# Optimization experiments

Measured on AMD Instinct MI355X. Metric: run time of the kernel, lower is better.

The kernel has to match this reference:

```python
import jax, jax.numpy as jnp
import numpy as np

DIM = 384
HEADS = 12
W = 7  # window_size
N = W * W
B = 4096

def _relative_position_index(ws):
    ch = np.arange(ws)
    coords = np.stack(np.meshgrid(ch, ch, indexing='ij'))  # [2, W, W]
    cf = coords.reshape(2, -1)  # [2, W*W]
    rel = cf[:, :, None] - cf[:, None, :]  # [2, N, N]
    rel = rel.transpose(1, 2, 0)
    rel[:, :, 0] += ws - 1
    rel[:, :, 1] += ws - 1
    rel[:, :, 0] *= 2 * ws - 1
    return rel.sum(-1).astype(np.int32)  # [N, N]

def setup_inputs() -> dict:
    key = jax.random.key(0)
    ks = jax.random.split(key, 8)
    s = 0.02
    return {
        'x': jax.random.normal(ks[0], (B, N, DIM), jnp.float32),
        'y': jax.random.normal(ks[1], (B, N, DIM), jnp.float32),
        'q_w': jax.random.normal(ks[2], (DIM, DIM), jnp.float32) * s,
        'q_b': jnp.zeros((DIM,), jnp.float32),
        'kv_w': jax.random.normal(ks[3], (2 * DIM, DIM), jnp.float32) * s,
        'kv_b': jnp.zeros((2 * DIM,), jnp.float32),
        'proj_w': jax.random.normal(ks[4], (DIM, DIM), jnp.float32) * s,
        'proj_b': jnp.zeros((DIM,), jnp.float32),
        'rel_table': jax.random.normal(ks[5], ((2 * W - 1) ** 2, HEADS), jnp.float32) * s,
        'rel_index': jnp.asarray(_relative_position_index(W)),
    }

def reference(x, y, q_w, q_b, kv_w, kv_b, proj_w, proj_b, rel_table, rel_index):
    Bx, N1, C = x.shape
    N2 = y.shape[1]
    hd = C // HEADS
    scale = hd ** -0.5
    # projections (torch Linear: x @ W^T + b)
    q = (x @ q_w.T + q_b).reshape(Bx, N1, HEADS, hd)
    kv = (y @ kv_w.T + kv_b).reshape(Bx, N2, 2, HEADS, hd)
    k = kv[:, :, 0]  # [B, N2, H, d]
    v = kv[:, :, 1]
    attn = jnp.einsum('bqhd,bkhd->bhqk', q, k) * scale
    # relative position bias: [N1, N2, H] -> [H, N1, N2]
    bias = rel_table[rel_index.reshape(-1)].reshape(N1, N2, HEADS)
    attn = attn + jnp.transpose(bias, (2, 0, 1))[None]
    attn = jax.nn.softmax(attn, axis=-1)
    out = jnp.einsum('bhqk,bkhd->bqhd', attn, v).reshape(Bx, N1, C)
    return out @ proj_w.T + proj_b
```

## Files before the change

### kernel.cpp

```cpp
#include <hip/hip_runtime.h>

#define DIM 384
#define HEADS 12
#define HD 32
#define NTOK 49
#define NWIN 4096
#define MTOT (NWIN*NTOK)
#define PSTR 72

typedef __attribute__((ext_vector_type(8))) __bf16 bf16x8;
typedef __attribute__((ext_vector_type(4))) float f32x4;

static __device__ __forceinline__ f32x4 mfma16(bf16x8 a, bf16x8 b, f32x4 c) {
  return __builtin_amdgcn_mfma_f32_16x16x32_bf16(a, b, c, 0, 0, 0);
}

static __device__ __forceinline__ void gload_lds16(const void* g, void* l) {
  __builtin_amdgcn_global_load_lds(
      (const __attribute__((address_space(1))) unsigned int*)g,
      (__attribute__((address_space(3))) unsigned int*)l, 16, 0, 0);
}

__global__ void k_prep(const float* __restrict__ qw, const float* __restrict__ kvw,
                       const float* __restrict__ pw, const float* __restrict__ rel_table,
                       const int* __restrict__ rel_index,
                       __bf16* __restrict__ qw_bf, __bf16* __restrict__ kvw_bf,
                       __bf16* __restrict__ pw_bf, float* __restrict__ bias_pad) {
  int i = blockIdx.x * 256 + threadIdx.x;
  if (i < DIM*DIM)   qw_bf[i] = (__bf16)qw[i];
  if (i < 2*DIM*DIM) kvw_bf[i] = (__bf16)kvw[i];
  if (i < DIM*DIM)   pw_bf[i] = (__bf16)pw[i];
  if (i < HEADS*64*64) {
    int h = i >> 12, rem = i & 4095, q = rem >> 6, k = rem & 63;
    float v;
    if (k >= NTOK)      v = -1e30f;
    else if (q >= NTOK) v = 0.0f;
    else v = rel_table[rel_index[q*NTOK + k] * HEADS + h];
    bias_pad[i] = v;
  }
}

__global__ __launch_bounds__(256) void k_cvt(const float* __restrict__ x,
                                             const float* __restrict__ y,
                                             __bf16* __restrict__ xb,
                                             __bf16* __restrict__ yb) {
  const size_t NCH = (size_t)MTOT * DIM / 8;
  size_t i = (size_t)blockIdx.x * 256 + threadIdx.x;
  size_t stride = (size_t)gridDim.x * 256;
  for (; i < 2*NCH; i += stride) {
    const float* s; __bf16* d; size_t c;
    if (i < NCH) { s = x; d = xb; c = i; } else { s = y; d = yb; c = i - NCH; }
    float4 v0 = *(const float4*)(s + c*8);
    float4 v1 = *(const float4*)(s + c*8 + 4);
    bf16x8 t;
    t[0]=(__bf16)v0.x; t[1]=(__bf16)v0.y; t[2]=(__bf16)v0.z; t[3]=(__bf16)v0.w;
    t[4]=(__bf16)v1.x; t[5]=(__bf16)v1.y; t[6]=(__bf16)v1.z; t[7]=(__bf16)v1.w;
    *(bf16x8*)(d + c*8) = t;
  }
}

__global__ __launch_bounds__(256, 4) void k_qkv(
    const __bf16* __restrict__ xb, const __bf16* __restrict__ yb,
    const __bf16* __restrict__ qw_bf, const __bf16* __restrict__ kvw_bf,
    const float* __restrict__ q_b, const float* __restrict__ kv_b,
    __bf16* __restrict__ Qws, __bf16* __restrict__ Kws, __bf16* __restrict__ Vws)
{
  int b = blockIdx.x;
  int orig = (b & 7) * 1764 + (b >> 3);
  int mtile = orig / 9;
  int nt9 = orig - mtile*9;
  const __bf16* A; const __bf16* Bw; const float* bias; __bf16* Cout;
  int wrow0, col0;
  if (nt9 < 3) { A = xb; Bw = qw_bf; bias = q_b; Cout = Qws; wrow0 = nt9*128; col0 = wrow0; }
  else {
    A = yb; Bw = kvw_bf; bias = kv_b; wrow0 = (nt9-3)*128;
    if (wrow0 < DIM) { Cout = Kws; col0 = wrow0; } else { Cout = Vws; col0 = wrow0 - DIM; }
  }
  bias += wrow0;

  __shared__ __align__(16) __bf16 As[2][128*32];
  __shared__ __align__(16) __bf16 Bs[2][128*32];

  int t = threadIdx.x, lane = t & 63, wave = t >> 6;
  int l15 = lane & 15, g = lane >> 4;
  int wr = (wave >> 1) * 64, wc = (wave & 1) * 64;
  int row0b = mtile*128;

  int sr  = 2*(lane >> 3) + ((lane >> 2) & 1);
  int scb = (lane & 3) ^ ((lane >> 3) & 3);
  const __bf16* asrc[2]; const __bf16* bsrc[2];
  #pragma unroll
  for (int j = 0; j < 2; ++j) {
    int ar = (wave*2 + j)*16 + sr;
    asrc[j] = A  + (size_t)(row0b + ar)*DIM + scb*8;
    bsrc[j] = Bw + (size_t)(wrow0 + ar)*DIM + scb*8;
  }

  f32x4 acc[4][4];
  #pragma unroll
  for (int a=0;a<4;a++)
    #pragma unroll
    for (int bb=0;bb<4;bb++) acc[a][bb] = (f32x4){0.f,0.f,0.f,0.f};

  #pragma unroll
  for (int j = 0; j < 2; ++j) {
    gload_lds16(asrc[j], (char*)&As[0][0] + (wave*2+j)*1024);
    gload_lds16(bsrc[j], (char*)&Bs[0][0] + (wave*2+j)*1024);
  }
  __syncthreads();

  int lslot = l15*64 + ((g ^ ((l15 >> 1) & 3)) << 4);

  int buf = 0;
  #pragma unroll 2
  for (int kt = 0; kt < 12; ++kt) {
    if (kt < 11) {
      int kk = (kt+1)*32;
      #pragma unroll
      for (int j = 0; j < 2; ++j) {
        gload_lds16(asrc[j] + kk, (char*)&As[buf^1][0] + (wave*2+j)*1024);
        gload_lds16(bsrc[j] + kk, (char*)&Bs[buf^1][0] + (wave*2+j)*1024);
      }
    }
    bf16x8 af[4], bfv[4];
    #pragma unroll
    for (int a=0;a<4;a++)
      af[a]  = *(const bf16x8*)((const char*)&As[buf][0] + (wr + a*16)*64 + lslot);
    #pragma unroll
    for (int bb=0;bb<4;bb++)
      bfv[bb] = *(const bf16x8*)((const char*)&Bs[buf][0] + (wc + bb*16)*64 + lslot);
    #pragma unroll
    for (int a=0;a<4;a++)
      #pragma unroll
      for (int bb=0;bb<4;bb++)
        acc[a][bb] = mfma16(af[a], bfv[bb], acc[a][bb]);
    __syncthreads();
    buf ^= 1;
  }

  #pragma unroll
  for (int a=0;a<4;a++) {
    #pragma unroll
    for (int bb=0;bb<4;bb++) {
      int colw = wc + bb*16 + l15;
      float bi = bias[colw];
      size_t cbase = (size_t)(row0b + wr + a*16 + 4*g)*DIM + (col0 + colw);
      #pragma unroll
      for (int r=0;r<4;r++)
        Cout[cbase + (size_t)r*DIM] = (__bf16)(acc[a][bb][r] + bi);
    }
  }
}

__global__ __launch_bounds__(256) void k_attn(
    __bf16* qao,
    const __bf16* __restrict__ Kws, const __bf16* __restrict__ Vws,
    const float* __restrict__ bias_pad)
{
  __shared__ __align__(16) __bf16 Psh[4][64*PSTR];
  __shared__ __align__(16) __bf16 VTsh[4][32*PSTR];
  int b = blockIdx.x;
  int lane = threadIdx.x & 63, wave = threadIdx.x >> 6;
  int l15 = lane & 15, g = lane >> 4;
  __bf16* Pw  = Psh[wave];
  __bf16* VTw = VTsh[wave];
  size_t rowbase = (size_t)b * NTOK * DIM;
  const float scale = 0.17677669529663687f;

  for (int e = lane; e < 32*15; e += 64) {
    int d = e / 15, k = 49 + (e - d*15);
    VTw[d*PSTR + k] = (__bf16)0.0f;
  }

  for (int hh = 0; hh < 3; hh++) {
    int h = wave + hh*4;
    for (int e = lane; e < NTOK*HD; e += 64) {
      int k = e >> 5, d = e & 31;
      VTw[d*PSTR + k] = Vws[rowbase + (size_t)k*DIM + h*HD + d];
    }
    bf16x8 qf[4], kf[4];
    #pragma unroll
    for (int mt=0; mt<4; mt++) {
      int q = 16*mt + l15; if (q > 48) q = 48;
      qf[mt] = *(const bf16x8*)(qao + rowbase + (size_t)q*DIM + h*HD + g*8);
    }
    #pragma unroll
    for (int nt=0; nt<4; nt++) {
      int kk = 16*nt + l15; if (kk > 48) kk = 48;
      kf[nt] = *(const bf16x8*)(Kws + rowbase + (size_t)kk*DIM + h*HD + g*8);
    }
    f32x4 sacc[4][4];
    #pragma unroll
    for (int mt=0; mt<4; mt++)
      #pragma unroll
      for (int nt=0; nt<4; nt++)
        sacc[mt][nt] = mfma16(qf[mt], kf[nt], (f32x4){0.f,0.f,0.f,0.f});

    const float* bt = bias_pad + h*4096;
    float rs[4][4];
    #pragma unroll
    for (int mt=0; mt<4; mt++) {
      #pragma unroll
      for (int r=0; r<4; r++) {
        int q = 16*mt + 4*g + r;
        float v0 = sacc[mt][0][r]*scale + bt[q*64 +  0 + l15];
        float v1 = sacc[mt][1][r]*scale + bt[q*64 + 16 + l15];
        float v2 = sacc[mt][2][r]*scale + bt[q*64 + 32 + l15];
        float v3 = sacc[mt][3][r]*scale + bt[q*64 + 48 + l15];
        float m = fmaxf(fmaxf(v0,v1), fmaxf(v2,v3));
        #pragma unroll
        for (int off=1; off<16; off<<=1) m = fmaxf(m, __shfl_xor(m, off));
        v0 = __expf(v0-m); v1 = __expf(v1-m); v2 = __expf(v2-m); v3 = __expf(v3-m);
        float s = v0+v1+v2+v3;
        #pragma unroll
        for (int off=1; off<16; off<<=1) s += __shfl_xor(s, off);
        rs[mt][r] = s;
        Pw[q*PSTR +  0 + l15] = (__bf16)v0;
        Pw[q*PSTR + 16 + l15] = (__bf16)v1;
        Pw[q*PSTR + 32 + l15] = (__bf16)v2;
        Pw[q*PSTR + 48 + l15] = (__bf16)v3;
      }
    }

    #pragma unroll
    for (int mt=0; mt<4; mt++) {
      #pragma unroll
      for (int dt=0; dt<2; dt++) {
        f32x4 o = (f32x4){0.f,0.f,0.f,0.f};
        #pragma unroll
        for (int ks=0; ks<2; ks++) {
          bf16x8 pa = *(const bf16x8*)(Pw  + (16*mt + l15)*PSTR + 32*ks + 8*g);
          bf16x8 vb = *(const bf16x8*)(VTw + (16*dt + l15)*PSTR + 32*ks + 8*g);
          o = mfma16(pa, vb, o);
        }
        #pragma unroll
        for (int r=0; r<4; r++) {
          int q = 16*mt + 4*g + r;
          if (q < NTOK)
            qao[rowbase + (size_t)q*DIM + h*HD + 16*dt + l15] = (__bf16)(o[r] / rs[mt][r]);
        }
      }
    }
  }
}

__global__ __launch_bounds__(256, 4) void k_proj(
    const __bf16* __restrict__ Aao, const __bf16* __restrict__ pw_bf,
    const float* __restrict__ pb, float* __restrict__ out)
{
  int b = blockIdx.x;
  int orig = (b & 7) * 588 + (b >> 3);
  int mtile = orig / 3;
  int nt = orig - mtile*3;
  int lane = threadIdx.x & 63, wave = threadIdx.x >> 6;
  int l15 = lane & 15, g = lane >> 4;
  int wr = (wave >> 1) * 64, wc = (wave & 1) * 64;
  int row0b = mtile*128;
  int col00 = nt*128;

  __shared__ __align__(16) __bf16 As[2][128*32];
  __shared__ __align__(16) __bf16 Bs[2][128*32];

  int sr  = 2*(lane >> 3) + ((lane >> 2) & 1);
  int scb = (lane & 3) ^ ((lane >> 3) & 3);
  const __bf16* asrc[2]; const __bf16* bsrc[2];
  #pragma unroll
  for (int j = 0; j < 2; ++j) {
    int ar = (wave*2 + j)*16 + sr;
    asrc[j] = Aao   + (size_t)(row0b + ar)*DIM + scb*8;
    bsrc[j] = pw_bf + (size_t)(col00 + ar)*DIM + scb*8;
  }

  f32x4 acc[4][4];
  #pragma unroll
  for (int a=0;a<4;a++)
    #pragma unroll
    for (int bb=0;bb<4;bb++) acc[a][bb] = (f32x4){0.f,0.f,0.f,0.f};

  #pragma unroll
  for (int j = 0; j < 2; ++j) {
    gload_lds16(asrc[j], (char*)&As[0][0] + (wave*2+j)*1024);
    gload_lds16(bsrc[j], (char*)&Bs[0][0] + (wave*2+j)*1024);
  }
  __syncthreads();

  int lslot = l15*64 + ((g ^ ((l15 >> 1) & 3)) << 4);

  int buf = 0;
  #pragma unroll 2
  for (int kt = 0; kt < 12; ++kt) {
    if (kt < 11) {
      int kk = (kt+1)*32;
      #pragma unroll
      for (int j = 0; j < 2; ++j) {
        gload_lds16(asrc[j] + kk, (char*)&As[buf^1][0] + (wave*2+j)*1024);
        gload_lds16(bsrc[j] + kk, (char*)&Bs[buf^1][0] + (wave*2+j)*1024);
      }
    }
    bf16x8 af[4], bfv[4];
    #pragma unroll
    for (int a=0;a<4;a++)
      af[a]  = *(const bf16x8*)((const char*)&As[buf][0] + (wr + a*16)*64 + lslot);
    #pragma unroll
    for (int bb=0;bb<4;bb++)
      bfv[bb] = *(const bf16x8*)((const char*)&Bs[buf][0] + (wc + bb*16)*64 + lslot);
    #pragma unroll
    for (int a=0;a<4;a++)
      #pragma unroll
      for (int bb=0;bb<4;bb++)
        acc[a][bb] = mfma16(af[a], bfv[bb], acc[a][bb]);
    __syncthreads();
    buf ^= 1;
  }

  #pragma unroll
  for (int a=0;a<4;a++) {
    #pragma unroll
    for (int bb=0;bb<4;bb++) {
      int col = col00 + wc + bb*16 + l15;
      float bi = pb[col];
      size_t cbase = (size_t)(row0b + wr + a*16 + 4*g)*DIM + col;
      #pragma unroll
      for (int r=0;r<4;r++)
        out[cbase + (size_t)r*DIM] = acc[a][bb][r] + bi;
    }
  }
}

extern "C" void kernel_launch(void* const* d_in, const int* in_sizes, int n_in,
                              void* d_out, int out_size, void* d_ws, size_t ws_size,
                              hipStream_t stream)
{
  const float* x   = (const float*)d_in[0];
  const float* y   = (const float*)d_in[1];
  const float* qw  = (const float*)d_in[2];
  const float* qb  = (const float*)d_in[3];
  const float* kvw = (const float*)d_in[4];
  const float* kvb = (const float*)d_in[5];
  const float* pw  = (const float*)d_in[6];
  const float* pb  = (const float*)d_in[7];
  const float* rt  = (const float*)d_in[8];
  const int*   ri  = (const int*)d_in[9];
  float* out = (float*)d_out;

  char* ws = (char*)d_ws;
  const size_t WS_NEEDED = 1376256ull + 3ull*154140672ull;
  if (ws_size < WS_NEEDED) return;

  __bf16* qw_bf    = (__bf16*)(ws);
  __bf16* kvw_bf   = (__bf16*)(ws + 294912);
  __bf16* pw_bf    = (__bf16*)(ws + 884736);
  float*  bias_pad = (float*)(ws + 1179648);
  __bf16* Qws      = (__bf16*)(ws + 1376256);
  __bf16* Kws      = Qws + (size_t)MTOT*DIM;
  __bf16* Vws      = Kws + (size_t)MTOT*DIM;

  __bf16* xb = (__bf16*)d_out;
  __bf16* yb = xb + (size_t)MTOT*DIM;

  k_prep<<<dim3(1152), dim3(256), 0, stream>>>(qw, kvw, pw, rt, ri, qw_bf, kvw_bf, pw_bf, bias_pad);
  k_cvt <<<dim3(4096), dim3(256), 0, stream>>>(x, y, xb, yb);
  k_qkv <<<dim3(1568*9), dim3(256), 0, stream>>>(xb, yb, qw_bf, kvw_bf, qb, kvb, Qws, Kws, Vws);
  k_attn<<<dim3(NWIN), dim3(256), 0, stream>>>(Qws, Kws, Vws, bias_pad);
  k_proj<<<dim3(1568*3), dim3(256), 0, stream>>>(Qws, pw_bf, pb, out);
}
```

Before: 950.9 us.

## Fuse fp32-to-bf16 input conversion into QKV GEMM A-tile loading

Removes the separate conversion kernel that wrote bf16 copies of x and y, and has the QKV GEMM load fp32 A tiles through registers, convert them, and store them into swizzled LDS. The full-tensor write and reread of the bf16 intermediates and one kernel launch go away. In exchange each A tile is fetched as fp32 once per output column tile, doubling A-side bytes. It also replaces async global-to-LDS loads with register-staged loads whose LDS store happens after the MFMAs.

Result: faster. 863.7 us (-9.2%).

```diff
diff --git a/kernel.cpp b/kernel.cpp
--- a/kernel.cpp
+++ b/kernel.cpp
@@ -19,6 +19,13 @@
   __builtin_amdgcn_global_load_lds(
       (const __attribute__((address_space(1))) unsigned int*)g,
       (__attribute__((address_space(3))) unsigned int*)l, 16, 0, 0);
+}
+
+static __device__ __forceinline__ bf16x8 cvt8(float4 v0, float4 v1) {
+  bf16x8 t;
+  t[0]=(__bf16)v0.x; t[1]=(__bf16)v0.y; t[2]=(__bf16)v0.z; t[3]=(__bf16)v0.w;
+  t[4]=(__bf16)v1.x; t[5]=(__bf16)v1.y; t[6]=(__bf16)v1.z; t[7]=(__bf16)v1.w;
+  return t;
 }
 
 __global__ void k_prep(const float* __restrict__ qw, const float* __restrict__ kvw,
@@ -40,27 +47,8 @@
   }
 }
 
-__global__ __launch_bounds__(256) void k_cvt(const float* __restrict__ x,
-                                             const float* __restrict__ y,
-                                             __bf16* __restrict__ xb,
-                                             __bf16* __restrict__ yb) {
-  const size_t NCH = (size_t)MTOT * DIM / 8;
-  size_t i = (size_t)blockIdx.x * 256 + threadIdx.x;
-  size_t stride = (size_t)gridDim.x * 256;
-  for (; i < 2*NCH; i += stride) {
-    const float* s; __bf16* d; size_t c;
-    if (i < NCH) { s = x; d = xb; c = i; } else { s = y; d = yb; c = i - NCH; }
-    float4 v0 = *(const float4*)(s + c*8);
-    float4 v1 = *(const float4*)(s + c*8 + 4);
-    bf16x8 t;
-    t[0]=(__bf16)v0.x; t[1]=(__bf16)v0.y; t[2]=(__bf16)v0.z; t[3]=(__bf16)v0.w;
-    t[4]=(__bf16)v1.x; t[5]=(__bf16)v1.y; t[6]=(__bf16)v1.z; t[7]=(__bf16)v1.w;
-    *(bf16x8*)(d + c*8) = t;
-  }
-}
-
 __global__ __launch_bounds__(256, 4) void k_qkv(
-    const __bf16* __restrict__ xb, const __bf16* __restrict__ yb,
+    const float* __restrict__ x, const float* __restrict__ y,
     const __bf16* __restrict__ qw_bf, const __bf16* __restrict__ kvw_bf,
     const float* __restrict__ q_b, const float* __restrict__ kv_b,
     __bf16* __restrict__ Qws, __bf16* __restrict__ Kws, __bf16* __restrict__ Vws)
@@ -69,11 +57,11 @@
   int orig = (b & 7) * 1764 + (b >> 3);
   int mtile = orig / 9;
   int nt9 = orig - mtile*9;
-  const __bf16* A; const __bf16* Bw; const float* bias; __bf16* Cout;
+  const float* A; const __bf16* Bw; const float* bias; __bf16* Cout;
   int wrow0, col0;
-  if (nt9 < 3) { A = xb; Bw = qw_bf; bias = q_b; Cout = Qws; wrow0 = nt9*128; col0 = wrow0; }
+  if (nt9 < 3) { A = x; Bw = qw_bf; bias = q_b; Cout = Qws; wrow0 = nt9*128; col0 = wrow0; }
   else {
-    A = yb; Bw = kvw_bf; bias = kv_b; wrow0 = (nt9-3)*128;
+    A = y; Bw = kvw_bf; bias = kv_b; wrow0 = (nt9-3)*128;
     if (wrow0 < DIM) { Cout = Kws; col0 = wrow0; } else { Cout = Vws; col0 = wrow0 - DIM; }
   }
   bias += wrow0;
@@ -86,15 +74,18 @@
   int wr = (wave >> 1) * 64, wc = (wave & 1) * 64;
   int row0b = mtile*128;
 
+  int srow = t >> 1, sh = t & 1;
+  const float* asrc = A + (size_t)(row0b + srow)*DIM + sh*16;
+  int swk = (srow >> 1) & 3;
+  unsigned lds_a0 = srow*64 + ((( (2*sh)   ) ^ swk) << 4);
+  unsigned lds_a1 = srow*64 + ((( (2*sh)|1 ) ^ swk) << 4);
+
   int sr  = 2*(lane >> 3) + ((lane >> 2) & 1);
   int scb = (lane & 3) ^ ((lane >> 3) & 3);
-  const __bf16* asrc[2]; const __bf16* bsrc[2];
-  #pragma unroll
-  for (int j = 0; j < 2; ++j) {
-    int ar = (wave*2 + j)*16 + sr;
-    asrc[j] = A  + (size_t)(row0b + ar)*DIM + scb*8;
-    bsrc[j] = Bw + (size_t)(wrow0 + ar)*DIM + scb*8;
-  }
+  const __bf16* bsrc[2];
+  #pragma unroll
+  for (int j = 0; j < 2; ++j)
+    bsrc[j] = Bw + (size_t)(wrow0 + (wave*2 + j)*16 + sr)*DIM + scb*8;
 
   f32x4 acc[4][4];
   #pragma unroll
@@ -102,11 +93,14 @@
     #pragma unroll
     for (int bb=0;bb<4;bb++) acc[a][bb] = (f32x4){0.f,0.f,0.f,0.f};
 
-  #pragma unroll
-  for (int j = 0; j < 2; ++j) {
-    gload_lds16(asrc[j], (char*)&As[0][0] + (wave*2+j)*1024);
+  float4 r0, r1, r2, r3;
+  r0 = *(const float4*)(asrc);     r1 = *(const float4*)(asrc + 4);
+  r2 = *(const float4*)(asrc + 8); r3 = *(const float4*)(asrc + 12);
+  #pragma unroll
+  for (int j = 0; j < 2; ++j)
     gload_lds16(bsrc[j], (char*)&Bs[0][0] + (wave*2+j)*1024);
-  }
+  *(bf16x8*)((char*)&As[0][0] + lds_a0) = cvt8(r0, r1);
+  *(bf16x8*)((char*)&As[0][0] + lds_a1) = cvt8(r2, r3);
   __syncthreads();
 
   int lslot = l15*64 + ((g ^ ((l15 >> 1) & 3)) << 4);
@@ -116,11 +110,11 @@
   for (int kt = 0; kt < 12; ++kt) {
     if (kt < 11) {
       int kk = (kt+1)*32;
-      #pragma unroll
-      for (int j = 0; j < 2; ++j) {
-        gload_lds16(asrc[j] + kk, (char*)&As[buf^1][0] + (wave*2+j)*1024);
+      r0 = *(const float4*)(asrc + kk);     r1 = *(const float4*)(asrc + kk + 4);
+      r2 = *(const float4*)(asrc + kk + 8); r3 = *(const float4*)(asrc + kk + 12);
+      #pragma unroll
+      for (int j = 0; j < 2; ++j)
         gload_lds16(bsrc[j] + kk, (char*)&Bs[buf^1][0] + (wave*2+j)*1024);
-      }
     }
     bf16x8 af[4], bfv[4];
     #pragma unroll
@@ -134,6 +128,10 @@
       #pragma unroll
       for (int bb=0;bb<4;bb++)
         acc[a][bb] = mfma16(af[a], bfv[bb], acc[a][bb]);
+    if (kt < 11) {
+      *(bf16x8*)((char*)&As[buf^1][0] + lds_a0) = cvt8(r0, r1);
+      *(bf16x8*)((char*)&As[buf^1][0] + lds_a1) = cvt8(r2, r3);
+    }
     __syncthreads();
     buf ^= 1;
   }
@@ -355,12 +353,8 @@
   __bf16* Kws      = Qws + (size_t)MTOT*DIM;
   __bf16* Vws      = Kws + (size_t)MTOT*DIM;
 
-  __bf16* xb = (__bf16*)d_out;
-  __bf16* yb = xb + (size_t)MTOT*DIM;
-
   k_prep<<<dim3(1152), dim3(256), 0, stream>>>(qw, kvw, pw, rt, ri, qw_bf, kvw_bf, pw_bf, bias_pad);
-  k_cvt <<<dim3(4096), dim3(256), 0, stream>>>(x, y, xb, yb);
-  k_qkv <<<dim3(1568*9), dim3(256), 0, stream>>>(xb, yb, qw_bf, kvw_bf, qb, kvb, Qws, Kws, Vws);
+  k_qkv <<<dim3(1568*9), dim3(256), 0, stream>>>(x, y, qw_bf, kvw_bf, qb, kvb, Qws, Kws, Vws);
   k_attn<<<dim3(NWIN), dim3(256), 0, stream>>>(Qws, Kws, Vws, bias_pad);
   k_proj<<<dim3(1568*3), dim3(256), 0, stream>>>(Qws, pw_bf, pb, out);
 }
```
